# Kernel optimization log

Hardware: AMD Instinct MI355X
Metric: run time of the kernel (lower is better)

The kernel has to match this reference:

```python
import jax, jax.numpy as jnp
import numpy as np

MSG_DIM = 100
REG_WEIGHT = 1.0
N_NODES = 100000
N_EDGES = 1000000
D_FEAT = 6
HIDDEN = 300
OUT_DIM = 2


def setup_inputs() -> dict:
    key = jax.random.key(0)
    ks = jax.random.split(key, 10)
    def glorot(k, shape):
        fan_in = shape[0]
        return jax.random.normal(k, shape, dtype=jnp.float32) / jnp.sqrt(jnp.float32(fan_in))
    return {
        "x": jax.random.normal(ks[0], (N_NODES, D_FEAT), dtype=jnp.float32),
        "edge_index": jax.random.randint(ks[1], (2, N_EDGES), 0, N_NODES, dtype=jnp.int64)
            if jax.config.jax_enable_x64 else jax.random.randint(ks[1], (2, N_EDGES), 0, N_NODES, dtype=jnp.int32),
        "y": jax.random.normal(ks[2], (N_NODES, OUT_DIM), dtype=jnp.float32),
        "target": jax.random.normal(ks[3], (N_NODES, OUT_DIM), dtype=jnp.float32),
        "W1": glorot(ks[4], (2 * D_FEAT, HIDDEN)),
        "b1": jnp.zeros((HIDDEN,), dtype=jnp.float32),
        "W2": glorot(ks[5], (HIDDEN, HIDDEN)),
        "b2": jnp.zeros((HIDDEN,), dtype=jnp.float32),
        "W3": glorot(ks[6], (HIDDEN, 2 * MSG_DIM)),
        "b3": jnp.zeros((2 * MSG_DIM,), dtype=jnp.float32),
    }


def reference(x, edge_index, y, target, W1, b1, W2, b2, W3, b3):
    # MAE term: sum |y - target| / n_nodes
    base_loss = jnp.sum(jnp.abs(y - target)) / y.shape[0]
    # Gather sender/receiver node features per edge and concat -> [E, 2*d_feat]
    e = jnp.concatenate([x[edge_index[0]], x[edge_index[1]]], axis=1)
    # edge_model MLP: 2*d_feat -> 300 -> 300 -> 2*msg_dim
    h = jax.nn.relu(e @ W1 + b1)
    h = jax.nn.relu(h @ W2 + b2)
    messages = h @ W3 + b3  # [E, 2*msg_dim]
    mu = messages[:, :MSG_DIM]
    logvar = messages[:, MSG_DIM:]
    kl_reg = jnp.sum(0.5 * (mu * mu + jnp.exp(logvar) - logvar - 1.0)) / messages.shape[0]
    return base_loss + REG_WEIGHT * kl_reg
```

## Files before the change

### kernel.cpp

```cpp
#include <hip/hip_runtime.h>

#define N_NODES 100000
#define N_EDGES 1000000
#define D_FEAT  6
#define HIDDEN  300
#define HID_P   320
#define MSG     100
#define OUTC    200
#define OUTC_P  208
#define MT      64
#define NT_H    (HID_P/16)
#define NT_M    13
#define KS_H    (HID_P/32)
#define NPART   (N_EDGES/MT)
#define LOG2E   1.44269504f
#define LN2     0.69314718f

typedef __bf16 bf16_t;
typedef __bf16 bf16x8 __attribute__((ext_vector_type(8)));
typedef __bf16 bf16x4 __attribute__((ext_vector_type(4)));
typedef __bf16 bf16x2 __attribute__((ext_vector_type(2)));
typedef float  floatx4 __attribute__((ext_vector_type(4)));

#define PREP_BLOCKS 700
#define LOSS_BLOCKS 200
__global__ void prep_kernel(const float* __restrict__ W1, const float* __restrict__ W2,
                            const float* __restrict__ W3, bf16_t* __restrict__ W1P,
                            bf16_t* __restrict__ W2P, bf16_t* __restrict__ W3P,
                            const float* __restrict__ y, const float* __restrict__ t,
                            float* __restrict__ out) {
    if (blockIdx.x >= PREP_BLOCKS) {
        float s = 0.f;
        for (int i = (blockIdx.x - PREP_BLOCKS) * blockDim.x + threadIdx.x;
             i < N_NODES * 2; i += LOSS_BLOCKS * blockDim.x)
            s += fabsf(y[i] - t[i]);
        #pragma unroll
        for (int off = 32; off; off >>= 1) s += __shfl_down(s, off);
        __shared__ float red[4];
        if ((threadIdx.x & 63) == 0) red[threadIdx.x >> 6] = s;
        __syncthreads();
        if (threadIdx.x == 0)
            atomicAdd(out, (red[0] + red[1] + red[2] + red[3]) * (1.0f / N_NODES));
        return;
    }
    const int n1 = NT_H * 512;
    const int n2 = NT_H * KS_H * 512;
    const int n3 = NT_M * KS_H * 512;
    const int total = n1 + n2 + n3;
    for (int id = blockIdx.x * blockDim.x + threadIdx.x; id < total;
         id += PREP_BLOCKS * blockDim.x) {
        if (id < n1) {
            int nt = id >> 9, rem = id & 511, lane = rem >> 3, j = rem & 7;
            int n = nt * 16 + (lane & 15), k = (lane >> 4) * 8 + j;
            float v = (n < HIDDEN && k < 2 * D_FEAT) ? W1[k * HIDDEN + n] : 0.f;
            W1P[id] = (bf16_t)v;
        } else if (id < n1 + n2) {
            int r = id - n1;
            int chunk = r >> 9, rem = r & 511, lane = rem >> 3, j = rem & 7;
            int ks = chunk % KS_H, nt = chunk / KS_H;
            int n = nt * 16 + (lane & 15), k = ks * 32 + (lane >> 4) * 8 + j;
            float v = (n < HIDDEN && k < HIDDEN) ? W2[k * HIDDEN + n] : 0.f;
            W2P[r] = (bf16_t)v;
        } else {
            int r = id - n1 - n2;
            int chunk = r >> 9, rem = r & 511, lane = rem >> 3, j = rem & 7;
            int ks = chunk % KS_H, nt = chunk / KS_H;
            int n = nt * 16 + (lane & 15), k = ks * 32 + (lane >> 4) * 8 + j;
            float v = (n < OUTC && k < HIDDEN) ? W3[k * OUTC + n] : 0.f;
            if (n >= MSG) v *= LOG2E;
            W3P[r] = (bf16_t)v;
        }
    }
}

#define RED_BLOCKS 64
__global__ void reduce_kernel(const float* __restrict__ part, float* __restrict__ out) {
    float s = 0.f;
    for (int i = blockIdx.x * blockDim.x + threadIdx.x; i < NPART;
         i += RED_BLOCKS * blockDim.x)
        s += part[i];
    #pragma unroll
    for (int off = 32; off; off >>= 1) s += __shfl_down(s, off);
    __shared__ float red[4];
    if ((threadIdx.x & 63) == 0) red[threadIdx.x >> 6] = s;
    __syncthreads();
    if (threadIdx.x == 0)
        atomicAdd(out, (red[0] + red[1] + red[2] + red[3]) * (0.5f / N_EDGES));
}

static __device__ __forceinline__ floatx4 mfma16(bf16x8 a, bf16x8 b, floatx4 c) {
    return __builtin_amdgcn_mfma_f32_16x16x32_bf16(a, b, c, 0, 0, 0);
}

template<int KSN, int SE>
__device__ __forceinline__ void gemm5x4(
    const bf16_t* __restrict__ Wbase0,
    const bf16_t* __restrict__ Hsrc, int lane,
    const floatx4 (&binit)[5], floatx4 (&acc)[5][4]) {
    #pragma unroll
    for (int i = 0; i < 5; i++)
        #pragma unroll
        for (int e = 0; e < 4; e++) acc[i][e] = binit[i];
    const bf16_t* Wb = Wbase0 + lane * 8;
    const bf16_t* Hb = Hsrc + lane * 8;
    #pragma unroll 2
    for (int ks = 0; ks < KSN; ks++) {
        bf16x8 hb0 = *(const bf16x8*)(Hb + ks * 512);
        bf16x8 hb1 = *(const bf16x8*)(Hb + ks * 512 + SE);
        bf16x8 hb2 = *(const bf16x8*)(Hb + ks * 512 + 2 * SE);
        bf16x8 hb3 = *(const bf16x8*)(Hb + ks * 512 + 3 * SE);
        #pragma unroll
        for (int i = 0; i < 5; i++) {
            bf16x8 wf = *(const bf16x8*)(Wb + i * (KSN * 512) + ks * 512);
            acc[i][0] = mfma16(wf, hb0, acc[i][0]);
            acc[i][1] = mfma16(wf, hb1, acc[i][1]);
            acc[i][2] = mfma16(wf, hb2, acc[i][2]);
            acc[i][3] = mfma16(wf, hb3, acc[i][3]);
        }
    }
}

__device__ __forceinline__ void epi5(
    bf16_t* __restrict__ Hf, int w, int q, int l16, const floatx4 (&acc)[5][4]) {
    #pragma unroll
    for (int i = 0; i < 5; i++) {
        int n0 = (5 * w + i) * 16 + 4 * q;
        int ks = n0 >> 5, lp = l16 + 16 * ((n0 >> 3) & 3), j0 = n0 & 7;
        #pragma unroll
        for (int e = 0; e < 4; e++) {
            bf16x4 pk;
            #pragma unroll
            for (int r = 0; r < 4; r++)
                pk[r] = (bf16_t)fmaxf(acc[i][e][r], 0.f);
            *(bf16x4*)&Hf[((e * KS_H + ks) * 64 + lp) * 8 + j0] = pk;
        }
    }
}

__global__ __launch_bounds__(256, 3) void mlp_kernel(
    const float* __restrict__ x, const int* __restrict__ ei,
    const bf16_t* __restrict__ W1P, const bf16_t* __restrict__ W2P,
    const bf16_t* __restrict__ W3P,
    const float* __restrict__ b1, const float* __restrict__ b2,
    const float* __restrict__ b3, float* __restrict__ part) {
    __shared__ __align__(16) bf16_t A1f[4 * 64 * 8];
    __shared__ __align__(16) bf16_t Hf[4 * KS_H * 64 * 8];
    __shared__ float red[4];

    const int tid  = threadIdx.x;
    const int w    = tid >> 6, lane = tid & 63;
    const int q    = lane >> 4, l16 = lane & 15;
    const long e0 = (long)blockIdx.x * MT;

    bf16x8 wf1[5];
    floatx4 bv1[5], bv2[5];
    #pragma unroll
    for (int i = 0; i < 5; i++) {
        wf1[i] = *(const bf16x8*)&W1P[((5 * w + i) * 64 + lane) * 8];
        int n0 = (5 * w + i) * 16 + 4 * q;
        bv1[i] = (n0 < HIDDEN) ? *(const floatx4*)&b1[n0] : (floatx4){0.f, 0.f, 0.f, 0.f};
        bv2[i] = (n0 < HIDDEN) ? *(const floatx4*)&b2[n0] : (floatx4){0.f, 0.f, 0.f, 0.f};
    }

    if (tid < 2 * MT) {
        int m = tid >> 1, side = tid & 1;
        int node = ei[(long)side * N_EDGES + e0 + m];
        const float2* xr = (const float2*)(x + (long)node * D_FEAT);
        float2 v0 = xr[0], v1 = xr[1], v2 = xr[2];
        int et = m >> 4, ml = m & 15;
        bf16_t* Ab = &A1f[(et * 64 + ml) * 8];
        if (side == 0) {
            bf16x4 lo = {(bf16_t)v0.x, (bf16_t)v0.y, (bf16_t)v1.x, (bf16_t)v1.y};
            *(bf16x4*)&Ab[0] = lo;
            bf16x2 mid = {(bf16_t)v2.x, (bf16_t)v2.y};
            *(bf16x2*)&Ab[4] = mid;
        } else {
            bf16x2 hi2 = {(bf16_t)v0.x, (bf16_t)v0.y};
            *(bf16x2*)&Ab[6] = hi2;
            bf16x8 top = {(bf16_t)v1.x, (bf16_t)v1.y, (bf16_t)v2.x, (bf16_t)v2.y,
                          (bf16_t)0.f, (bf16_t)0.f, (bf16_t)0.f, (bf16_t)0.f};
            *(bf16x8*)&A1f[(et * 64 + ml + 16) * 8] = top;
        }
    } else {
        int idx = tid - 128;
        int et = idx >> 5, lr = 32 + (idx & 31);
        bf16x8 z = {};
        *(bf16x8*)&A1f[(et * 64 + lr) * 8] = z;
    }
    __syncthreads();

    floatx4 acc[5][4];

    {
        bf16x8 hb0 = *(const bf16x8*)&A1f[lane * 8];
        bf16x8 hb1 = *(const bf16x8*)&A1f[(64 + lane) * 8];
        bf16x8 hb2 = *(const bf16x8*)&A1f[(128 + lane) * 8];
        bf16x8 hb3 = *(const bf16x8*)&A1f[(192 + lane) * 8];
        #pragma unroll
        for (int i = 0; i < 5; i++) {
            acc[i][0] = mfma16(wf1[i], hb0, bv1[i]);
            acc[i][1] = mfma16(wf1[i], hb1, bv1[i]);
            acc[i][2] = mfma16(wf1[i], hb2, bv1[i]);
            acc[i][3] = mfma16(wf1[i], hb3, bv1[i]);
        }
    }
    epi5(Hf, w, q, l16, acc);
    __syncthreads();

    gemm5x4<KS_H, KS_H * 512>(W2P + (5 * w) * (KS_H * 512), Hf, lane, bv2, acc);
    __syncthreads();
    epi5(Hf, w, q, l16, acc);
    __syncthreads();

    floatx4 a3[3][4], aq;
    const int n0q = 192 + 4 * q;
    {
        #pragma unroll
        for (int t = 0; t < 3; t++) {
            int n0 = (3 * w + t) * 16 + 4 * q;
            floatx4 bv = *(const floatx4*)&b3[n0];
            if (n0 >= MSG) bv = bv * LOG2E;
            #pragma unroll
            for (int e = 0; e < 4; e++) a3[t][e] = bv;
        }
        aq = (n0q < OUTC) ? *(const floatx4*)&b3[n0q] * LOG2E
                          : (floatx4){0.f, 0.f, 0.f, 0.f};
    }
    {
        const bf16_t* W3b = W3P + (3 * w) * (KS_H * 512) + lane * 8;
        const bf16_t* Wqb = W3P + 12 * (KS_H * 512) + lane * 8;
        const bf16_t* Hb  = Hf + lane * 8;
        const bf16_t* Hq  = Hf + w * (KS_H * 512) + lane * 8;
        #pragma unroll 2
        for (int ks = 0; ks < KS_H; ks++) {
            bf16x8 hb0 = *(const bf16x8*)(Hb + ks * 512);
            bf16x8 hb1 = *(const bf16x8*)(Hb + ks * 512 + KS_H * 512);
            bf16x8 hb2 = *(const bf16x8*)(Hb + ks * 512 + 2 * KS_H * 512);
            bf16x8 hb3 = *(const bf16x8*)(Hb + ks * 512 + 3 * KS_H * 512);
            #pragma unroll
            for (int t = 0; t < 3; t++) {
                bf16x8 wf = *(const bf16x8*)(W3b + t * (KS_H * 512) + ks * 512);
                a3[t][0] = mfma16(wf, hb0, a3[t][0]);
                a3[t][1] = mfma16(wf, hb1, a3[t][1]);
                a3[t][2] = mfma16(wf, hb2, a3[t][2]);
                a3[t][3] = mfma16(wf, hb3, a3[t][3]);
            }
            bf16x8 wq = *(const bf16x8*)(Wqb + ks * 512);
            bf16x8 hq = *(const bf16x8*)(Hq + ks * 512);
            aq = mfma16(wq, hq, aq);
        }
    }
    float sm = 0.f, se = 0.f, svp = 0.f, cnt = 0.f;
    #pragma unroll
    for (int t = 0; t < 3; t++) {
        int n0 = (3 * w + t) * 16 + 4 * q;
        if (n0 < MSG) {
            #pragma unroll
            for (int e = 0; e < 4; e++)
                #pragma unroll
                for (int r = 0; r < 4; r++) {
                    float v = a3[t][e][r];
                    sm += v * v;
                }
        } else {
            #pragma unroll
            for (int e = 0; e < 4; e++)
                #pragma unroll
                for (int r = 0; r < 4; r++) {
                    float v = a3[t][e][r];
                    se += __builtin_exp2f(v);
                    svp += v;
                }
            cnt += 16.f;
        }
    }
    if (n0q < OUTC) {
        #pragma unroll
        for (int r = 0; r < 4; r++) {
            float v = aq[r];
            se += __builtin_exp2f(v);
            svp += v;
        }
        cnt += 4.f;
    }
    float s = sm + se - svp * LN2 - cnt;
    #pragma unroll
    for (int off = 32; off; off >>= 1) s += __shfl_down(s, off);
    if (lane == 0) red[w] = s;
    __syncthreads();
    if (tid == 0)
        part[blockIdx.x] = red[0] + red[1] + red[2] + red[3];
}

extern "C" void kernel_launch(void* const* d_in, const int* in_sizes, int n_in,
                              void* d_out, int out_size, void* d_ws, size_t ws_size,
                              hipStream_t stream) {
    const float* x      = (const float*)d_in[0];
    const int*   ei     = (const int*)d_in[1];
    const float* y      = (const float*)d_in[2];
    const float* target = (const float*)d_in[3];
    const float* W1     = (const float*)d_in[4];
    const float* b1     = (const float*)d_in[5];
    const float* W2     = (const float*)d_in[6];
    const float* b2     = (const float*)d_in[7];
    const float* W3     = (const float*)d_in[8];
    const float* b3     = (const float*)d_in[9];
    float* out = (float*)d_out;

    bf16_t* W1P = (bf16_t*)d_ws;
    bf16_t* W2P = W1P + NT_H * 512;
    bf16_t* W3P = W2P + NT_H * KS_H * 512;
    float*  part = (float*)(W3P + NT_M * KS_H * 512);

    hipMemsetAsync(d_out, 0, sizeof(float), stream);
    prep_kernel<<<PREP_BLOCKS + LOSS_BLOCKS, 256, 0, stream>>>(
        W1, W2, W3, W1P, W2P, W3P, y, target, out);
    mlp_kernel<<<N_EDGES / MT, 256, 0, stream>>>(x, ei, W1P, W2P, W3P, b1, b2, b3, part);
    reduce_kernel<<<RED_BLOCKS, 256, 0, stream>>>(part, out);
}
```

Before: 409.3 us.

## Give each wave its own 16-edge tile across layers 2 and 3, dropping barriers

Layers 2 and 3 change from splitting output columns across waves (with all four edge tiles shared through LDS) to each wave owning one 16-edge tile and computing all output columns. This removes the __syncthreads between layer 2, its epilogue and layer 3, because each wave writes and reads only its own Hf slice. The cost is that every wave now streams the full W2 and W3 from global memory/cache (four times more weight traffic per block) with ks loops not unrolled, and each weight fragment is reused only once instead of across four edge tiles.

Measured after the change: 760.3 us. 1.86x slower.

```diff
diff --git a/kernel.cpp b/kernel.cpp
--- a/kernel.cpp
+++ b/kernel.cpp
@@ -92,34 +92,6 @@
     return __builtin_amdgcn_mfma_f32_16x16x32_bf16(a, b, c, 0, 0, 0);
 }
 
-template<int KSN, int SE>
-__device__ __forceinline__ void gemm5x4(
-    const bf16_t* __restrict__ Wbase0,
-    const bf16_t* __restrict__ Hsrc, int lane,
-    const floatx4 (&binit)[5], floatx4 (&acc)[5][4]) {
-    #pragma unroll
-    for (int i = 0; i < 5; i++)
-        #pragma unroll
-        for (int e = 0; e < 4; e++) acc[i][e] = binit[i];
-    const bf16_t* Wb = Wbase0 + lane * 8;
-    const bf16_t* Hb = Hsrc + lane * 8;
-    #pragma unroll 2
-    for (int ks = 0; ks < KSN; ks++) {
-        bf16x8 hb0 = *(const bf16x8*)(Hb + ks * 512);
-        bf16x8 hb1 = *(const bf16x8*)(Hb + ks * 512 + SE);
-        bf16x8 hb2 = *(const bf16x8*)(Hb + ks * 512 + 2 * SE);
-        bf16x8 hb3 = *(const bf16x8*)(Hb + ks * 512 + 3 * SE);
-        #pragma unroll
-        for (int i = 0; i < 5; i++) {
-            bf16x8 wf = *(const bf16x8*)(Wb + i * (KSN * 512) + ks * 512);
-            acc[i][0] = mfma16(wf, hb0, acc[i][0]);
-            acc[i][1] = mfma16(wf, hb1, acc[i][1]);
-            acc[i][2] = mfma16(wf, hb2, acc[i][2]);
-            acc[i][3] = mfma16(wf, hb3, acc[i][3]);
-        }
-    }
-}
-
 __device__ __forceinline__ void epi5(
     bf16_t* __restrict__ Hf, int w, int q, int l16, const floatx4 (&acc)[5][4]) {
     #pragma unroll
@@ -153,13 +125,12 @@
     const long e0 = (long)blockIdx.x * MT;
 
     bf16x8 wf1[5];
-    floatx4 bv1[5], bv2[5];
+    floatx4 bv1[5];
     #pragma unroll
     for (int i = 0; i < 5; i++) {
         wf1[i] = *(const bf16x8*)&W1P[((5 * w + i) * 64 + lane) * 8];
         int n0 = (5 * w + i) * 16 + 4 * q;
         bv1[i] = (n0 < HIDDEN) ? *(const floatx4*)&b1[n0] : (floatx4){0.f, 0.f, 0.f, 0.f};
-        bv2[i] = (n0 < HIDDEN) ? *(const floatx4*)&b2[n0] : (floatx4){0.f, 0.f, 0.f, 0.f};
     }
 
     if (tid < 2 * MT) {
@@ -189,9 +160,8 @@
     }
     __syncthreads();
 
-    floatx4 acc[5][4];
-
     {
+        floatx4 acc[5][4];
         bf16x8 hb0 = *(const bf16x8*)&A1f[lane * 8];
         bf16x8 hb1 = *(const bf16x8*)&A1f[(64 + lane) * 8];
         bf16x8 hb2 = *(const bf16x8*)&A1f[(128 + lane) * 8];
@@ -203,85 +173,82 @@
             acc[i][2] = mfma16(wf1[i], hb2, bv1[i]);
             acc[i][3] = mfma16(wf1[i], hb3, bv1[i]);
         }
-    }
-    epi5(Hf, w, q, l16, acc);
-    __syncthreads();
-
-    gemm5x4<KS_H, KS_H * 512>(W2P + (5 * w) * (KS_H * 512), Hf, lane, bv2, acc);
-    __syncthreads();
-    epi5(Hf, w, q, l16, acc);
-    __syncthreads();
-
-    floatx4 a3[3][4], aq;
-    const int n0q = 192 + 4 * q;
+        epi5(Hf, w, q, l16, acc);
+    }
+    __syncthreads();
+
+    floatx4 acc2[20];
+    #pragma unroll
+    for (int nt = 0; nt < 20; nt++) {
+        int n0 = nt * 16 + 4 * q;
+        acc2[nt] = (n0 < HIDDEN) ? *(const floatx4*)&b2[n0]
+                                 : (floatx4){0.f, 0.f, 0.f, 0.f};
+    }
     {
-        #pragma unroll
-        for (int t = 0; t < 3; t++) {
-            int n0 = (3 * w + t) * 16 + 4 * q;
-            floatx4 bv = *(const floatx4*)&b3[n0];
-            if (n0 >= MSG) bv = bv * LOG2E;
-            #pragma unroll
-            for (int e = 0; e < 4; e++) a3[t][e] = bv;
-        }
-        aq = (n0q < OUTC) ? *(const floatx4*)&b3[n0q] * LOG2E
-                          : (floatx4){0.f, 0.f, 0.f, 0.f};
+        const bf16_t* Wb  = W2P + lane * 8;
+        const bf16_t* Hbw = Hf + w * (KS_H * 512) + lane * 8;
+        #pragma unroll 1
+        for (int ks = 0; ks < KS_H; ks++) {
+            bf16x8 hb = *(const bf16x8*)(Hbw + ks * 512);
+            #pragma unroll
+            for (int nt = 0; nt < 20; nt++) {
+                bf16x8 wf = *(const bf16x8*)(Wb + (nt * KS_H + ks) * 512);
+                acc2[nt] = mfma16(wf, hb, acc2[nt]);
+            }
+        }
+    }
+    #pragma unroll
+    for (int nt = 0; nt < 20; nt++) {
+        int n0 = nt * 16 + 4 * q;
+        int ks = n0 >> 5, lp = l16 + 16 * ((n0 >> 3) & 3), j0 = n0 & 7;
+        bf16x4 pk;
+        #pragma unroll
+        for (int r = 0; r < 4; r++)
+            pk[r] = (bf16_t)fmaxf(acc2[nt][r], 0.f);
+        *(bf16x4*)&Hf[((w * KS_H + ks) * 64 + lp) * 8 + j0] = pk;
+    }
+
+    floatx4 acc3[13];
+    #pragma unroll
+    for (int nt = 0; nt < 13; nt++) {
+        int n0 = nt * 16 + 4 * q;
+        floatx4 bv = (n0 < OUTC) ? *(const floatx4*)&b3[n0]
+                                 : (floatx4){0.f, 0.f, 0.f, 0.f};
+        if (n0 >= MSG) bv = bv * LOG2E;
+        acc3[nt] = bv;
     }
     {
-        const bf16_t* W3b = W3P + (3 * w) * (KS_H * 512) + lane * 8;
-        const bf16_t* Wqb = W3P + 12 * (KS_H * 512) + lane * 8;
-        const bf16_t* Hb  = Hf + lane * 8;
-        const bf16_t* Hq  = Hf + w * (KS_H * 512) + lane * 8;
-        #pragma unroll 2
+        const bf16_t* Wb  = W3P + lane * 8;
+        const bf16_t* Hbw = Hf + w * (KS_H * 512) + lane * 8;
+        #pragma unroll 1
         for (int ks = 0; ks < KS_H; ks++) {
-            bf16x8 hb0 = *(const bf16x8*)(Hb + ks * 512);
-            bf16x8 hb1 = *(const bf16x8*)(Hb + ks * 512 + KS_H * 512);
-            bf16x8 hb2 = *(const bf16x8*)(Hb + ks * 512 + 2 * KS_H * 512);
-            bf16x8 hb3 = *(const bf16x8*)(Hb + ks * 512 + 3 * KS_H * 512);
-            #pragma unroll
-            for (int t = 0; t < 3; t++) {
-                bf16x8 wf = *(const bf16x8*)(W3b + t * (KS_H * 512) + ks * 512);
-                a3[t][0] = mfma16(wf, hb0, a3[t][0]);
-                a3[t][1] = mfma16(wf, hb1, a3[t][1]);
-                a3[t][2] = mfma16(wf, hb2, a3[t][2]);
-                a3[t][3] = mfma16(wf, hb3, a3[t][3]);
-            }
-            bf16x8 wq = *(const bf16x8*)(Wqb + ks * 512);
-            bf16x8 hq = *(const bf16x8*)(Hq + ks * 512);
-            aq = mfma16(wq, hq, aq);
+            bf16x8 hb = *(const bf16x8*)(Hbw + ks * 512);
+            #pragma unroll
+            for (int nt = 0; nt < 13; nt++) {
+                bf16x8 wf = *(const bf16x8*)(Wb + (nt * KS_H + ks) * 512);
+                acc3[nt] = mfma16(wf, hb, acc3[nt]);
+            }
         }
     }
     float sm = 0.f, se = 0.f, svp = 0.f, cnt = 0.f;
     #pragma unroll
-    for (int t = 0; t < 3; t++) {
-        int n0 = (3 * w + t) * 16 + 4 * q;
+    for (int nt = 0; nt < 13; nt++) {
+        int n0 = nt * 16 + 4 * q;
         if (n0 < MSG) {
             #pragma unroll
-            for (int e = 0; e < 4; e++)
-                #pragma unroll
-                for (int r = 0; r < 4; r++) {
-                    float v = a3[t][e][r];
-                    sm += v * v;
-                }
-        } else {
-            #pragma unroll
-            for (int e = 0; e < 4; e++)
-                #pragma unroll
-                for (int r = 0; r < 4; r++) {
-                    float v = a3[t][e][r];
-                    se += __builtin_exp2f(v);
-                    svp += v;
-                }
-            cnt += 16.f;
-        }
-    }
-    if (n0q < OUTC) {
-        #pragma unroll
-        for (int r = 0; r < 4; r++) {
-            float v = aq[r];
-            se += __builtin_exp2f(v);
-            svp += v;
-        }
-        cnt += 4.f;
+            for (int r = 0; r < 4; r++) {
+                float v = acc3[nt][r];
+                sm += v * v;
+            }
+        } else if (n0 < OUTC) {
+            #pragma unroll
+            for (int r = 0; r < 4; r++) {
+                float v = acc3[nt][r];
+                se += __builtin_exp2f(v);
+                svp += v;
+            }
+            cnt += 4.f;
+        }
     }
     float s = sm + se - svp * LN2 - cnt;
     #pragma unroll
```
